# Optimization experiments

Measured on AMD Instinct MI355X. Metric: run time of the kernel, lower is better.

## Reference

```python
import math
import jax, jax.numpy as jnp
import numpy as np

T = 4096          # sequence length
H = 2048          # hidden_size
I = 8192          # intermediate_size = 4*H
LAYER_ID = 1
N_LAYERS = 24
EPS = 1e-5        # layer_norm_epsilon


def setup_inputs() -> dict:
    key = jax.random.key(0)
    ks = jax.random.split(key, 8)
    s = 1.0 / math.sqrt(H)
    si = 1.0 / math.sqrt(I)
    r0 = LAYER_ID / (N_LAYERS - 1)          # ratio_0_to_1
    r1 = 1.0 - LAYER_ID / N_LAYERS          # ratio_1_to_almost_0
    h = jnp.arange(H, dtype=jnp.float32)
    x = h / H
    time_decay = -5.0 + 8.0 * (h / (H - 1)) ** (0.7 + 1.3 * r0)
    zigzag = 0.5 * ((jnp.arange(1, H + 1) % 3).astype(jnp.float32) - 1.0)
    time_first = jnp.full((H,), math.log(0.3), jnp.float32) + zigzag
    tm_key = x ** r1
    tm_value = tm_key + 0.3 * r0
    tm_recep = x ** (0.5 * r1)
    return {
        "hidden": jax.random.normal(ks[0], (T, H), jnp.float32),
        "att_sx": jnp.zeros((H,), jnp.float32),
        "att_aa": jnp.zeros((H,), jnp.float32),
        "att_bb": jnp.zeros((H,), jnp.float32),
        "att_pp": jnp.full((H,), -1e30, jnp.float32),  # log-space -inf init
        "ffd_sx": jnp.zeros((H,), jnp.float32),
        "ln1_scale": jnp.ones((H,), jnp.float32),
        "ln1_bias": jnp.zeros((H,), jnp.float32),
        "ln2_scale": jnp.ones((H,), jnp.float32),
        "ln2_bias": jnp.zeros((H,), jnp.float32),
        "time_decay": time_decay.astype(jnp.float32),
        "time_first": time_first,
        "tm_key": tm_key.astype(jnp.float32),
        "tm_value": tm_value.astype(jnp.float32),
        "tm_recep": tm_recep.astype(jnp.float32),
        "Wk": jax.random.normal(ks[1], (H, H), jnp.float32) * s,
        "Wv": jax.random.normal(ks[2], (H, H), jnp.float32) * s,
        "Wr": jax.random.normal(ks[3], (H, H), jnp.float32) * s,
        "Wo": jax.random.normal(ks[4], (H, H), jnp.float32) * s,
        "ffn_tm_key": (x ** r1).astype(jnp.float32),
        "ffn_tm_recep": (x ** (0.5 * r1)).astype(jnp.float32),
        "Wfk": jax.random.normal(ks[5], (H, I), jnp.float32) * s,
        "Wfr": jax.random.normal(ks[6], (H, H), jnp.float32) * s,
        "Wfv": jax.random.normal(ks[7], (I, H), jnp.float32) * si,
    }


def _ln(x, scale, bias):
    mu = jnp.mean(x, axis=-1, keepdims=True)
    var = jnp.mean(jnp.square(x - mu), axis=-1, keepdims=True)
    return (x - mu) * jax.lax.rsqrt(var + EPS) * scale + bias


def _block(hidden, att_sx, att_aa, att_bb, att_pp, ffd_sx,
           ln1_scale, ln1_bias, ln2_scale, ln2_bias,
           time_decay, time_first, tm_key, tm_value, tm_recep,
           Wk, Wv, Wr, Wo, ffn_tm_key, ffn_tm_recep, Wfk, Wfr, Wfv):
    # ---- attention (WKV) sub-block ----
    x1 = _ln(hidden, ln1_scale, ln1_bias)               # [T,H]
    c_x = jnp.concatenate((att_sx[None, :], x1[:-1, :]), axis=0)  # token shift
    kx = x1 * tm_key + c_x * (1.0 - tm_key)
    vx = x1 * tm_value + c_x * (1.0 - tm_value)
    rx = x1 * tm_recep + c_x * (1.0 - tm_recep)
    r = jax.nn.sigmoid(rx @ Wr)                         # [T,H]
    k = kx @ Wk
    v = vx @ Wv
    w_decay = -jnp.exp(time_decay)                      # [H]

    def step(carry, kv):
        aa, bb, pp = carry
        kk, vv = kv
        ww = time_first + kk
        p = jnp.maximum(pp, ww)
        e1 = jnp.exp(pp - p)
        e2 = jnp.exp(ww - p)
        out_t = (e1 * aa + e2 * vv) / (e1 * bb + e2)
        ww2 = w_decay + pp
        p2 = jnp.maximum(ww2, kk)
        e1b = jnp.exp(ww2 - p2)
        e2b = jnp.exp(kk - p2)
        return (e1b * aa + e2b * vv, e1b * bb + e2b, p2), out_t

    (aa, bb, pp), cx = jax.lax.scan(step, (att_aa, att_bb, att_pp), (k, v))
    attention = x1 + (r * cx) @ Wo                      # inner residual (as in source)
    hidden2 = hidden + attention

    # ---- feed-forward (channel-mix) sub-block ----
    x2 = _ln(hidden2, ln2_scale, ln2_bias)
    sx2 = jnp.concatenate((ffd_sx[None, :], x2[:-1, :]), axis=0)
    fk = x2 * ffn_tm_key + sx2 * (1.0 - ffn_tm_key)
    fr = x2 * ffn_tm_recep + sx2 * (1.0 - ffn_tm_recep)
    rr = jax.nn.sigmoid(fr @ Wfr)
    kk2 = jnp.square(jax.nn.relu(fk @ Wfk))             # [T,I]
    ffn = rr * (kk2 @ Wfv)
    out = hidden2 + ffn
    return out, x1[-1, :], aa, bb, pp, x2[-1, :]


def reference(hidden, att_sx, att_aa, att_bb, att_pp, ffd_sx,
              ln1_scale, ln1_bias, ln2_scale, ln2_bias,
              time_decay, time_first, tm_key, tm_value, tm_recep,
              Wk, Wv, Wr, Wo, ffn_tm_key, ffn_tm_recep, Wfk, Wfr, Wfv):
    return _block(hidden, att_sx, att_aa, att_bb, att_pp, ffd_sx,
                  ln1_scale, ln1_bias, ln2_scale, ln2_bias,
                  time_decay, time_first, tm_key, tm_value, tm_recep,
                  Wk, Wv, Wr, Wo, ffn_tm_key, ffn_tm_recep, Wfk, Wfr, Wfv)
```

## Files before the change

### kernel.cpp

```cpp
#include <hip/hip_runtime.h>

#define T_SEQ 4096
#define HD 2048
#define ID 8192
#define LN_EPS 1e-5f
#define NCH 64
#define CHL 64
#define CHSZ ((size_t)NCH * HD)

typedef __attribute__((ext_vector_type(4))) float f32x4;
typedef __attribute__((ext_vector_type(8))) short short8;
typedef __attribute__((ext_vector_type(8))) unsigned short ushort8v;
typedef __attribute__((ext_vector_type(4))) unsigned short ushort4v;

#define GLB(p) ((const __attribute__((address_space(1))) void*)(p))
#define LDSP(p) ((__attribute__((address_space(3))) void*)(p))

__device__ __forceinline__ unsigned short f2bf(float f) {
  union { float f; unsigned int u; } x; x.f = f;
  unsigned int r = x.u + 0x7fffu + ((x.u >> 16) & 1u);
  return (unsigned short)(r >> 16);
}
__device__ __forceinline__ float bf2f(unsigned short u) {
  union { unsigned int i; float f; } x; x.i = ((unsigned int)u) << 16;
  return x.f;
}

__global__ void k_wt(const float* __restrict__ W, unsigned short* __restrict__ Wt,
                     int Nfull, int k_base, int n_base, int Kout) {
  __shared__ float tile[64][65];
  int tx = threadIdx.x, ty = threadIdx.y;
  int n0 = blockIdx.x * 64, k0 = blockIdx.y * 64;
#pragma unroll
  for (int j = 0; j < 8; ++j) {
    int k = ty + 8 * j;
    tile[k][tx] = W[(size_t)(k_base + k0 + k) * Nfull + n_base + n0 + tx];
  }
  __syncthreads();
  ushort8v v;
#pragma unroll
  for (int q = 0; q < 8; ++q) v[q] = f2bf(tile[ty * 8 + q][tx]);
  *(ushort8v*)&Wt[(size_t)(n0 + tx) * Kout + k0 + ty * 8] = v;
}

__global__ void k_ln(const float* __restrict__ x, const float* __restrict__ sc,
                     const float* __restrict__ bi, unsigned short* __restrict__ y,
                     float* __restrict__ lastrow) {
  int row = blockIdx.x, tid = threadIdx.x;
  const float* xr = x + (size_t)row * HD;
  f32x4 v0 = *(const f32x4*)(xr + tid * 4);
  f32x4 v1 = *(const f32x4*)(xr + 1024 + tid * 4);
  float s = 0.f, s2 = 0.f;
#pragma unroll
  for (int q = 0; q < 4; ++q) { s += v0[q] + v1[q]; s2 += v0[q] * v0[q] + v1[q] * v1[q]; }
#pragma unroll
  for (int o = 32; o; o >>= 1) { s += __shfl_xor(s, o); s2 += __shfl_xor(s2, o); }
  __shared__ float red[8];
  int wv = tid >> 6;
  if ((tid & 63) == 0) { red[wv] = s; red[4 + wv] = s2; }
  __syncthreads();
  if (tid == 0) {
    float a = red[0] + red[1] + red[2] + red[3];
    float b = red[4] + red[5] + red[6] + red[7];
    float mu = a * (1.f / HD);
    float var = b * (1.f / HD) - mu * mu;
    red[0] = mu; red[1] = rsqrtf(var + LN_EPS);
  }
  __syncthreads();
  float mu = red[0], rs = red[1];
  f32x4 s0 = *(const f32x4*)(sc + tid * 4), s1 = *(const f32x4*)(sc + 1024 + tid * 4);
  f32x4 b0 = *(const f32x4*)(bi + tid * 4), b1 = *(const f32x4*)(bi + 1024 + tid * 4);
  float o0[4], o1[4];
  ushort4v y0, y1;
#pragma unroll
  for (int q = 0; q < 4; ++q) {
    o0[q] = (v0[q] - mu) * rs * s0[q] + b0[q];
    o1[q] = (v1[q] - mu) * rs * s1[q] + b1[q];
    y0[q] = f2bf(o0[q]); y1[q] = f2bf(o1[q]);
  }
  unsigned short* yr = y + (size_t)row * HD;
  *(ushort4v*)(yr + tid * 4) = y0;
  *(ushort4v*)(yr + 1024 + tid * 4) = y1;
  if (row == T_SEQ - 1) {
#pragma unroll
    for (int q = 0; q < 4; ++q) {
      lastrow[tid * 4 + q] = o0[q];
      lastrow[1024 + tid * 4 + q] = o1[q];
    }
  }
}

__global__ void k_mix_att(const unsigned short* __restrict__ x1, const float* __restrict__ sx,
                          const float* __restrict__ tk, const float* __restrict__ tv,
                          const float* __restrict__ tr,
                          unsigned short* __restrict__ kx, unsigned short* __restrict__ vx,
                          unsigned short* __restrict__ rx) {
  size_t idx = ((size_t)blockIdx.x * 256 + threadIdx.x) * 4;
  int h = (int)(idx & (HD - 1));
  ushort4v xu = *(const ushort4v*)(x1 + idx);
  f32x4 x, c;
#pragma unroll
  for (int q = 0; q < 4; ++q) x[q] = bf2f(xu[q]);
  if (idx >= HD) {
    ushort4v cu = *(const ushort4v*)(x1 + idx - HD);
#pragma unroll
    for (int q = 0; q < 4; ++q) c[q] = bf2f(cu[q]);
  } else {
    c = *(const f32x4*)(sx + h);
  }
  f32x4 a = *(const f32x4*)(tk + h);
  f32x4 b = *(const f32x4*)(tv + h);
  f32x4 r = *(const f32x4*)(tr + h);
  ushort4v ok, ov, orr;
#pragma unroll
  for (int q = 0; q < 4; ++q) {
    ok[q] = f2bf(x[q] * a[q] + c[q] * (1.f - a[q]));
    ov[q] = f2bf(x[q] * b[q] + c[q] * (1.f - b[q]));
    orr[q] = f2bf(x[q] * r[q] + c[q] * (1.f - r[q]));
  }
  *(ushort4v*)(kx + idx) = ok;
  *(ushort4v*)(vx + idx) = ov;
  *(ushort4v*)(rx + idx) = orr;
}

__global__ void k_mix_ffn(const unsigned short* __restrict__ x2, const float* __restrict__ sx,
                          const float* __restrict__ tk, const float* __restrict__ tr,
                          unsigned short* __restrict__ fk, unsigned short* __restrict__ fr) {
  size_t idx = ((size_t)blockIdx.x * 256 + threadIdx.x) * 4;
  int h = (int)(idx & (HD - 1));
  ushort4v xu = *(const ushort4v*)(x2 + idx);
  f32x4 x, c;
#pragma unroll
  for (int q = 0; q < 4; ++q) x[q] = bf2f(xu[q]);
  if (idx >= HD) {
    ushort4v cu = *(const ushort4v*)(x2 + idx - HD);
#pragma unroll
    for (int q = 0; q < 4; ++q) c[q] = bf2f(cu[q]);
  } else {
    c = *(const f32x4*)(sx + h);
  }
  f32x4 a = *(const f32x4*)(tk + h);
  f32x4 r = *(const f32x4*)(tr + h);
  ushort4v ok, orr;
#pragma unroll
  for (int q = 0; q < 4; ++q) {
    ok[q] = f2bf(x[q] * a[q] + c[q] * (1.f - a[q]));
    orr[q] = f2bf(x[q] * r[q] + c[q] * (1.f - r[q]));
  }
  *(ushort4v*)(fk + idx) = ok;
  *(ushort4v*)(fr + idx) = orr;
}

__global__ void k_scan1(const unsigned short* __restrict__ kb,
                        const unsigned short* __restrict__ vb,
                        const float* __restrict__ td, float* __restrict__ scr) {
  int c = blockIdx.x >> 3;
  int h = (blockIdx.x & 7) * 256 + threadIdx.x;
  float wd = -__expf(td[h]);
  float a = 0.f, b = 0.f, p = -1e30f;
  size_t base = (size_t)c * CHL * HD + h;
#pragma unroll 4
  for (int u = 0; u < CHL; ++u) {
    float kk = bf2f(kb[base]), vv = bf2f(vb[base]);
    base += HD;
    float ww2 = wd + p;
    float p2 = fmaxf(ww2, kk);
    float e1 = __expf(ww2 - p2), e2 = __expf(kk - p2);
    a = e1 * a + e2 * vv;
    b = e1 * b + e2;
    p = p2;
  }
  size_t i = (size_t)c * HD + h;
  scr[i] = a;
  scr[CHSZ + i] = b;
  scr[2 * CHSZ + i] = p;
}

__global__ void k_scan2(const float* __restrict__ scr, float* __restrict__ stscr,
                        const float* __restrict__ aa0, const float* __restrict__ bb0,
                        const float* __restrict__ pp0, const float* __restrict__ td,
                        float* __restrict__ st) {
  int h = blockIdx.x * 256 + threadIdx.x;
  float aa = aa0[h], bb = bb0[h], pp = pp0[h];
  float wdL = -__expf(td[h]) * (float)CHL;
  for (int c = 0; c < NCH; ++c) {
    size_t i = (size_t)c * HD + h;
    stscr[i] = aa;
    stscr[CHSZ + i] = bb;
    stscr[2 * CHSZ + i] = pp;
    float ca = scr[i], cb = scr[CHSZ + i], cp = scr[2 * CHSZ + i];
    float ww2 = wdL + pp;
    float p2 = fmaxf(ww2, cp);
    float e1 = __expf(ww2 - p2), e2 = __expf(cp - p2);
    aa = e1 * aa + e2 * ca;
    bb = e1 * bb + e2 * cb;
    pp = p2;
  }
  st[HD + h] = aa;
  st[2 * HD + h] = bb;
  st[3 * HD + h] = pp;
}

__global__ void k_scan3(const unsigned short* __restrict__ kb,
                        const unsigned short* __restrict__ vb,
                        const unsigned short* __restrict__ rb,
                        const float* __restrict__ tf_, const float* __restrict__ td,
                        const float* __restrict__ stscr, unsigned short* __restrict__ rcx) {
  int c = blockIdx.x >> 3;
  int h = (blockIdx.x & 7) * 256 + threadIdx.x;
  size_t i0 = (size_t)c * HD + h;
  float aa = stscr[i0], bb = stscr[CHSZ + i0], pp = stscr[2 * CHSZ + i0];
  float tf = tf_[h];
  float wd = -__expf(td[h]);
  size_t base = (size_t)c * CHL * HD + h;
#pragma unroll 4
  for (int u = 0; u < CHL; ++u) {
    float kk = bf2f(kb[base]), vv = bf2f(vb[base]), rv = bf2f(rb[base]);
    float ww = tf + kk;
    float p = fmaxf(pp, ww);
    float e1 = __expf(pp - p), e2 = __expf(ww - p);
    float cx = (e1 * aa + e2 * vv) / (e1 * bb + e2);
    rcx[base] = f2bf(rv * cx);
    float ww2 = wd + pp;
    float p2 = fmaxf(ww2, kk);
    float e1b = __expf(ww2 - p2), e2b = __expf(kk - p2);
    aa = e1b * aa + e2b * vv;
    bb = e1b * bb + e2b;
    pp = p2;
    base += HD;
  }
}

__global__ void k_fvred(float* __restrict__ out, const unsigned short* __restrict__ rr,
                        const unsigned short* __restrict__ p0,
                        const unsigned short* __restrict__ p1) {
  size_t i = ((size_t)blockIdx.x * 256 + threadIdx.x) * 4;
  f32x4 o = *(f32x4*)(out + i);
  ushort4v r = *(const ushort4v*)(rr + i);
  ushort4v a = *(const ushort4v*)(p0 + i);
  ushort4v b = *(const ushort4v*)(p1 + i);
#pragma unroll
  for (int q = 0; q < 4; ++q) o[q] += bf2f(r[q]) * (bf2f(a[q]) + bf2f(b[q]));
  *(f32x4*)(out + i) = o;
}

#define MFMA_Q(mh, nh, bset)                                                   \
  _Pragma("unroll") for (int i_ = 0; i_ < 4; ++i_)                             \
  _Pragma("unroll") for (int j_ = 0; j_ < 2; ++j_)                             \
  _Pragma("unroll") for (int ks_ = 0; ks_ < 2; ++ks_)                          \
    acc[(mh)*4 + i_][(nh)*2 + j_] = __builtin_amdgcn_mfma_f32_16x16x32_bf16(   \
        aS[i_ * 2 + ks_], bset[j_ * 2 + ks_], acc[(mh)*4 + i_][(nh)*2 + j_], 0, 0, 0);

#define RD_A(mh)                                                               \
  { const char* pa_ = Ab + arow0 + (mh)*8192;                                  \
    aS[0] = *(const short8*)(pa_ + 0 * 2048 + swz0);                           \
    aS[1] = *(const short8*)(pa_ + 0 * 2048 + swz1);                           \
    aS[2] = *(const short8*)(pa_ + 1 * 2048 + swz0);                           \
    aS[3] = *(const short8*)(pa_ + 1 * 2048 + swz1);                           \
    aS[4] = *(const short8*)(pa_ + 2 * 2048 + swz0);                           \
    aS[5] = *(const short8*)(pa_ + 2 * 2048 + swz1);                           \
    aS[6] = *(const short8*)(pa_ + 3 * 2048 + swz0);                           \
    aS[7] = *(const short8*)(pa_ + 3 * 2048 + swz1); }

#define RD_B(arr, nh)                                                          \
  { const char* pb_ = Bb + brow0 + (nh)*4096;                                  \
    arr[0] = *(const short8*)(pb_ + 0 * 2048 + swz0);                          \
    arr[1] = *(const short8*)(pb_ + 0 * 2048 + swz1);                          \
    arr[2] = *(const short8*)(pb_ + 1 * 2048 + swz0);                          \
    arr[3] = *(const short8*)(pb_ + 1 * 2048 + swz1); }

template <int EPI>
__global__ __launch_bounds__(512, 2) void k_gemm256(
    const unsigned short* __restrict__ A, const unsigned short* __restrict__ A1,
    const unsigned short* __restrict__ A2,
    const unsigned short* __restrict__ Bt, const unsigned short* __restrict__ Bt1,
    const unsigned short* __restrict__ Bt2,
    int M, int N, int K, int lda, int ldb,
    unsigned short* __restrict__ Cb, unsigned short* __restrict__ Cb1,
    unsigned short* __restrict__ Cb2) {
  int koff = 0;
  if (EPI == 10) {
    koff = blockIdx.z * K;
    if (blockIdx.z) Cb = Cb1;
  } else {
    if (blockIdx.z == 1) { A = A1; Bt = Bt1; Cb = Cb1; }
    else if (blockIdx.z == 2) { A = A2; Bt = Bt2; Cb = Cb2; }
  }
  __shared__ char lds[131072];
  int tid = threadIdx.x;
  int wid = tid >> 6, lane = tid & 63;
  int row_l = lane & 15, kg = lane >> 4;
  int warp_m = wid >> 2, warp_n = wid & 3;
  int m0 = blockIdx.x * 256, n0 = blockIdx.y * 256;

  f32x4 acc[8][4];
#pragma unroll
  for (int i = 0; i < 8; ++i)
#pragma unroll
    for (int j = 0; j < 4; ++j)
#pragma unroll
      for (int q = 0; q < 4; ++q) acc[i][j][q] = 0.f;

  int srow = tid >> 3;
  int schunk = (tid & 7) ^ (srow & 7);
  const unsigned short* Asrc = A + (size_t)(m0 + srow) * lda + koff + schunk * 8;
  const unsigned short* Bsrc = Bt + (size_t)(n0 + srow) * ldb + koff + schunk * 8;
  char* ldsw = lds + wid * 1024;

  auto STAGE_A = [&](int d, int kt) {
#pragma unroll
    for (int h = 0; h < 2; ++h) {
      const unsigned short* s = Asrc + (size_t)(h * 128) * lda + kt;
      char* dst = ldsw + d * 65536 + h * 16384;
      __builtin_amdgcn_global_load_lds(GLB(s), LDSP(dst), 16, 0, 0);
      __builtin_amdgcn_global_load_lds(GLB(s + (size_t)64 * lda), LDSP(dst + 8192), 16, 0, 0);
    }
  };
  auto STAGE_B = [&](int d, int kt) {
#pragma unroll
    for (int h = 0; h < 2; ++h) {
      const unsigned short* s = Bsrc + (size_t)(h * 128) * ldb + kt;
      char* dst = ldsw + d * 65536 + 32768 + h * 16384;
      __builtin_amdgcn_global_load_lds(GLB(s), LDSP(dst), 16, 0, 0);
      __builtin_amdgcn_global_load_lds(GLB(s + (size_t)64 * ldb), LDSP(dst + 8192), 16, 0, 0);
    }
  };

  int swz0 = ((kg) ^ (row_l & 7)) << 4;
  int swz1 = ((4 + kg) ^ (row_l & 7)) << 4;
  int arow0 = (warp_m * 128 + row_l) * 128;
  int brow0 = (warp_n * 64 + row_l) * 128;

  short8 aS[8], b0[4], b1[4];
  int nt = K >> 6;
  STAGE_A(0, 0);
  STAGE_B(0, 0);

#pragma unroll 1
  for (int t = 0; t < nt; ++t) {
    int d = t & 1;
    const char* Ab = lds + d * 65536;
    const char* Bb = lds + d * 65536 + 32768;
    bool pre = (t + 1 < nt);
    int kn = (t + 1) << 6;
    if (pre) {
      STAGE_A(d ^ 1, kn);
      asm volatile("s_waitcnt vmcnt(4)" ::: "memory");
    } else {
      asm volatile("s_waitcnt vmcnt(0)" ::: "memory");
    }
    __builtin_amdgcn_s_barrier();
    RD_A(0)
    RD_B(b0, 0)
    asm volatile("s_waitcnt lgkmcnt(0)" ::: "memory");
    __builtin_amdgcn_s_setprio(1);
    MFMA_Q(0, 0, b0)
    __builtin_amdgcn_s_setprio(0);
    __builtin_amdgcn_s_barrier();
    if (pre) STAGE_B(d ^ 1, kn);
    RD_B(b1, 1)
    asm volatile("s_waitcnt lgkmcnt(0)" ::: "memory");
    __builtin_amdgcn_s_setprio(1);
    MFMA_Q(0, 1, b1)
    __builtin_amdgcn_s_setprio(0);
    __builtin_amdgcn_s_barrier();
    RD_A(1)
    asm volatile("s_waitcnt lgkmcnt(0)" ::: "memory");
    __builtin_amdgcn_s_setprio(1);
    MFMA_Q(1, 1, b1)
    __builtin_amdgcn_s_setprio(0);
    __builtin_amdgcn_s_barrier();
    __builtin_amdgcn_s_setprio(1);
    MFMA_Q(1, 0, b0)
    __builtin_amdgcn_s_setprio(0);
    __builtin_amdgcn_s_barrier();
  }

#pragma unroll
  for (int i = 0; i < 8; ++i) {
#pragma unroll
    for (int j = 0; j < 4; ++j) {
#pragma unroll
      for (int q = 0; q < 4; ++q) {
        int r = m0 + warp_m * 128 + i * 16 + kg * 4 + q;
        int c = n0 + warp_n * 64 + j * 16 + row_l;
        size_t idx = (size_t)r * N + c;
        float val = acc[i][j][q];
        if (EPI == 2) { float t2 = val > 0.f ? val * val : 0.f; Cb[idx] = f2bf(t2); }
        if (EPI == 8) {
          float o = (blockIdx.z == 2) ? 1.f / (1.f + __expf(-val)) : val;
          Cb[idx] = f2bf(o);
        }
        if (EPI == 10) Cb[idx] = f2bf(val);
      }
    }
  }
}

template <int EPI, int SWAP>
__global__ __launch_bounds__(512) void k_gemmB(
    const unsigned short* __restrict__ A, const unsigned short* __restrict__ Bt,
    int M, int N, int K, int lda, float* __restrict__ C,
    unsigned short* __restrict__ Cb, const float* __restrict__ E0,
    const unsigned short* __restrict__ E1b, const unsigned short* __restrict__ E0b) {
  __shared__ char lds[147456];
  int tid = threadIdx.x;
  int wid = tid >> 6, lane = tid & 63;
  int row_l = lane & 15, kg = lane >> 4;
  int warp_m = wid >> 2, warp_n = wid & 3;
  int bm = SWAP ? blockIdx.y : blockIdx.x;
  int bn = SWAP ? blockIdx.x : blockIdx.y;
  int m0 = bm * 128, n0 = bn * 256;

  f32x4 acc[4][4];
#pragma unroll
  for (int i = 0; i < 4; ++i)
#pragma unroll
    for (int j = 0; j < 4; ++j)
#pragma unroll
      for (int q = 0; q < 4; ++q) acc[i][j][q] = 0.f;

  int srow = tid >> 3;
  int schunk = (tid & 7) ^ (srow & 7);
  const unsigned short* Asrc = A + (size_t)(m0 + srow) * lda + schunk * 8;
  const unsigned short* Bsrc = Bt + (size_t)(n0 + srow) * K + schunk * 8;
  int wsw = wid * 1024;

  auto STAGE_P1 = [&](int d, int kt) {
    char* base = lds + d * 49152;
    __builtin_amdgcn_global_load_lds(GLB(Asrc + kt), LDSP(base + wsw), 16, 0, 0);
    __builtin_amdgcn_global_load_lds(GLB(Asrc + (size_t)64 * lda + kt),
                                     LDSP(base + 8192 + wsw), 16, 0, 0);
    __builtin_amdgcn_global_load_lds(GLB(Bsrc + kt), LDSP(base + 16384 + wsw), 16, 0, 0);
  };
  auto STAGE_P2 = [&](int d, int kt) {
    char* base = lds + d * 49152;
#pragma unroll
    for (int h = 1; h < 4; ++h)
      __builtin_amdgcn_global_load_lds(GLB(Bsrc + (size_t)(h * 64) * K + kt),
                                       LDSP(base + 16384 + h * 8192 + wsw), 16, 0, 0);
  };

  int swz0 = ((kg) ^ (row_l & 7)) << 4;
  int swz1 = ((4 + kg) ^ (row_l & 7)) << 4;
  int arow0 = (warp_m * 64 + row_l) * 128;
  int brow0 = (warp_n * 64 + row_l) * 128;

  short8 aS[8], b0[4], b1[4];
  int nt = K >> 6;
  STAGE_P1(0, 0); STAGE_P2(0, 0);
  STAGE_P1(1, 64); STAGE_P2(1, 64);

#pragma unroll 1
  for (int t = 0; t < nt; ++t) {
    int d = t % 3;
    const char* Ab = lds + d * 49152;
    const char* Bb = lds + d * 49152 + 16384;
    int b2 = t + 2 < nt ? (t + 2) % 3 : 0;
    int k2 = (t + 2) << 6;
    if (t + 2 < nt) {
      STAGE_P1(b2, k2);
      asm volatile("s_waitcnt vmcnt(9)" ::: "memory");
    } else if (t + 1 < nt) {
      asm volatile("s_waitcnt vmcnt(6)" ::: "memory");
    } else {
      asm volatile("s_waitcnt vmcnt(0)" ::: "memory");
    }
    __builtin_amdgcn_s_barrier();
    RD_A(0)
    RD_B(b0, 0)
    asm volatile("s_waitcnt lgkmcnt(0)" ::: "memory");
    __builtin_amdgcn_s_setprio(1);
    MFMA_Q(0, 0, b0)
    __builtin_amdgcn_s_setprio(0);
    __builtin_amdgcn_s_barrier();
    if (t + 2 < nt) STAGE_P2(b2, k2);
    RD_B(b1, 1)
    asm volatile("s_waitcnt lgkmcnt(0)" ::: "memory");
    __builtin_amdgcn_s_setprio(1);
    MFMA_Q(0, 1, b1)
    __builtin_amdgcn_s_setprio(0);
    __builtin_amdgcn_s_barrier();
  }

#pragma unroll
  for (int i = 0; i < 4; ++i) {
#pragma unroll
    for (int j = 0; j < 4; ++j) {
#pragma unroll
      for (int q = 0; q < 4; ++q) {
        int r = m0 + warp_m * 64 + i * 16 + kg * 4 + q;
        int c = n0 + warp_n * 64 + j * 16 + row_l;
        size_t idx = (size_t)r * N + c;
        float val = acc[i][j][q];
        if (EPI == 3) C[idx] = val + E0[idx] + bf2f(E1b[idx]);
        if (EPI == 6) Cb[idx] = f2bf(1.f / (1.f + __expf(-val)));
        if (EPI == 7) C[idx] += bf2f(E0b[idx]) * val;
      }
    }
  }
}

extern "C" void kernel_launch(void* const* d_in, const int* in_sizes, int n_in,
                              void* d_out, int out_size, void* d_ws, size_t ws_size,
                              hipStream_t stream) {
  (void)in_sizes; (void)n_in; (void)out_size;
  const float* hidden     = (const float*)d_in[0];
  const float* att_sx     = (const float*)d_in[1];
  const float* att_aa     = (const float*)d_in[2];
  const float* att_bb     = (const float*)d_in[3];
  const float* att_pp     = (const float*)d_in[4];
  const float* ffd_sx     = (const float*)d_in[5];
  const float* ln1_s      = (const float*)d_in[6];
  const float* ln1_b      = (const float*)d_in[7];
  const float* ln2_s      = (const float*)d_in[8];
  const float* ln2_b      = (const float*)d_in[9];
  const float* time_decay = (const float*)d_in[10];
  const float* time_first = (const float*)d_in[11];
  const float* tm_key     = (const float*)d_in[12];
  const float* tm_value   = (const float*)d_in[13];
  const float* tm_recep   = (const float*)d_in[14];
  const float* Wk         = (const float*)d_in[15];
  const float* Wv         = (const float*)d_in[16];
  const float* Wr         = (const float*)d_in[17];
  const float* Wo         = (const float*)d_in[18];
  const float* ffn_tm_key = (const float*)d_in[19];
  const float* ffn_tm_rec = (const float*)d_in[20];
  const float* Wfk        = (const float*)d_in[21];
  const float* Wfr        = (const float*)d_in[22];
  const float* Wfv        = (const float*)d_in[23];
  float* out = (float*)d_out;
  float* st = out + (size_t)T_SEQ * HD;

  const size_t MB8 = (size_t)HD * HD * 2;
  const size_t PG = (size_t)T_SEQ * HD * 2;
  char* w = (char*)d_ws;
  unsigned short* s0 = (unsigned short*)(w);
  unsigned short* s1 = (unsigned short*)(w + MB8);
  unsigned short* s2 = (unsigned short*)(w + 2 * MB8);
  unsigned short* s3 = (unsigned short*)(w + 3 * MB8);
  char* pA = w + 4 * MB8;
  char* pB = pA + PG;
  char* pC = pB + PG;
  char* pD = pC + PG;
  char* pE = pD + PG;
  char* pF = pE + PG;

  unsigned short* kx   = (unsigned short*)pA;
  unsigned short* vx   = (unsigned short*)pB;
  unsigned short* rx   = (unsigned short*)pC;
  unsigned short* kbf  = (unsigned short*)pD;
  unsigned short* x1bf = (unsigned short*)pE;
  unsigned short* vbf  = (unsigned short*)pF;
  unsigned short* rbf  = (unsigned short*)out;
  unsigned short* rcx  = (unsigned short*)pC;
  unsigned short* x2bf = (unsigned short*)pD;
  unsigned short* fk   = (unsigned short*)pF;
  unsigned short* fr   = (unsigned short*)pB;
  unsigned short* rr   = (unsigned short*)pA;
  unsigned short* kk2  = (unsigned short*)pB;
  unsigned short* pfv0 = (unsigned short*)pF;
  unsigned short* pfv1 = (unsigned short*)(w + 4 * MB8 + 6 * PG);
  float* scr   = (float*)s0;
  float* stscr = (float*)s1;
  bool big_ws = ws_size >= (size_t)(4 * MB8 + 7 * PG);

  dim3 tb64(64, 8);
  dim3 wg64(HD / 64, HD / 64);
  dim3 gBs(HD / 256, T_SEQ / 128);

  k_wt<<<wg64, tb64, 0, stream>>>(Wk, s0, HD, 0, 0, HD);
  k_wt<<<wg64, tb64, 0, stream>>>(Wv, s1, HD, 0, 0, HD);
  k_wt<<<wg64, tb64, 0, stream>>>(Wr, s2, HD, 0, 0, HD);
  k_wt<<<wg64, tb64, 0, stream>>>(Wo, s3, HD, 0, 0, HD);
  k_ln<<<T_SEQ, 256, 0, stream>>>(hidden, ln1_s, ln1_b, x1bf, st);
  k_mix_att<<<T_SEQ * HD / 1024, 256, 0, stream>>>(x1bf, att_sx, tm_key, tm_value, tm_recep,
                                                   kx, vx, rx);
  k_gemm256<8><<<dim3(T_SEQ / 256, HD / 256, 3), 512, 0, stream>>>(
      kx, vx, rx, s0, s1, s2, T_SEQ, HD, HD, HD, HD, kbf, vbf, rbf);
  k_scan1<<<NCH * 8, 256, 0, stream>>>(kbf, vbf, time_decay, scr);
  k_scan2<<<HD / 256, 256, 0, stream>>>(scr, stscr, att_aa, att_bb, att_pp, time_decay, st);
  k_scan3<<<NCH * 8, 256, 0, stream>>>(kbf, vbf, rbf, time_first, time_decay, stscr, rcx);
  k_gemmB<3, 1><<<gBs, 512, 0, stream>>>(rcx, s3, T_SEQ, HD, HD, HD, out, nullptr,
                                         hidden, x1bf, nullptr);

  k_ln<<<T_SEQ, 256, 0, stream>>>(out, ln2_s, ln2_b, x2bf, st + 4 * HD);
  k_mix_ffn<<<T_SEQ * HD / 1024, 256, 0, stream>>>(x2bf, ffd_sx, ffn_tm_key, ffn_tm_rec,
                                                   fk, fr);
  k_wt<<<wg64, tb64, 0, stream>>>(Wfr, s3, HD, 0, 0, HD);
  k_gemmB<6, 1><<<gBs, 512, 0, stream>>>(fr, s3, T_SEQ, HD, HD, HD, nullptr, rr,
                                         nullptr, nullptr, nullptr);
  for (int q = 0; q < 4; ++q)
    k_wt<<<wg64, tb64, 0, stream>>>(Wfk, s0 + (size_t)q * 2048 * 2048, ID, 0, q * 2048, HD);
  k_gemm256<2><<<dim3(T_SEQ / 256, ID / 256), 512, 0, stream>>>(
      fk, nullptr, nullptr, s0, nullptr, nullptr, T_SEQ, ID, HD, HD, HD,
      kk2, nullptr, nullptr);
  for (int q = 0; q < 4; ++q)
    k_wt<<<dim3(HD / 64, HD / 64), tb64, 0, stream>>>(Wfv, s0 + (size_t)q * 2048, HD,
                                                      q * 2048, 0, ID);
  if (big_ws) {
    k_gemm256<10><<<dim3(T_SEQ / 256, HD / 256, 2), 512, 0, stream>>>(
        kk2, nullptr, nullptr, s0, nullptr, nullptr, T_SEQ, HD, ID / 2, ID, ID,
        pfv0, pfv1, nullptr);
    k_fvred<<<T_SEQ * HD / 1024, 256, 0, stream>>>(out, rr, pfv0, pfv1);
  } else {
    k_gemmB<7, 1><<<gBs, 512, 0, stream>>>(kk2, s0, T_SEQ, HD, ID, ID, out, nullptr,
                                           nullptr, nullptr, rr);
  }
}
```

Baseline: 657.1 us.

## Batch weight transposes, drop gemmB block swap, fold rr scaling into split-K epilogue

The separate per-weight transpose launches are merged into batched launches that select the matrix from blockIdx.z. The transpose write-back changes from a vectorised 8-element store to coalesced scalar stores. The gemmB grid stops swapping blocks, so blockIdx.x now indexes M. The rr gate multiply moves from the reduction kernel into the split-K GEMM epilogue, which removes one read stream from the reduction but rounds each product to bf16 before the two halves are summed.

```diff
diff --git a/kernel.cpp b/kernel.cpp
--- a/kernel.cpp
+++ b/kernel.cpp
@@ -10,7 +10,6 @@
 
 typedef __attribute__((ext_vector_type(4))) float f32x4;
 typedef __attribute__((ext_vector_type(8))) short short8;
-typedef __attribute__((ext_vector_type(8))) unsigned short ushort8v;
 typedef __attribute__((ext_vector_type(4))) unsigned short ushort4v;
 
 #define GLB(p) ((const __attribute__((address_space(1))) void*)(p))
@@ -26,8 +25,9 @@
   return x.f;
 }
 
-__global__ void k_wt(const float* __restrict__ W, unsigned short* __restrict__ Wt,
-                     int Nfull, int k_base, int n_base, int Kout) {
+__device__ __forceinline__ void wt_body(const float* __restrict__ W,
+                                        unsigned short* __restrict__ Wt,
+                                        int Nfull, int k_base, int n_base, int Kout) {
   __shared__ float tile[64][65];
   int tx = threadIdx.x, ty = threadIdx.y;
   int n0 = blockIdx.x * 64, k0 = blockIdx.y * 64;
@@ -37,10 +37,31 @@
     tile[k][tx] = W[(size_t)(k_base + k0 + k) * Nfull + n_base + n0 + tx];
   }
   __syncthreads();
-  ushort8v v;
-#pragma unroll
-  for (int q = 0; q < 8; ++q) v[q] = f2bf(tile[ty * 8 + q][tx]);
-  *(ushort8v*)&Wt[(size_t)(n0 + tx) * Kout + k0 + ty * 8] = v;
+#pragma unroll
+  for (int j = 0; j < 8; ++j) {
+    int n = ty + 8 * j;
+    Wt[(size_t)(n0 + n) * Kout + k0 + tx] = f2bf(tile[tx][n]);
+  }
+}
+
+__global__ void k_wt(const float* __restrict__ W, unsigned short* __restrict__ Wt) {
+  wt_body(W, Wt, HD, 0, 0, HD);
+}
+
+__global__ void k_wt4(const float* __restrict__ W0, const float* __restrict__ W1,
+                      const float* __restrict__ W2, const float* __restrict__ W3,
+                      unsigned short* __restrict__ T) {
+  const float* W = W0;
+  if (blockIdx.z == 1) W = W1;
+  else if (blockIdx.z == 2) W = W2;
+  else if (blockIdx.z == 3) W = W3;
+  wt_body(W, T + (size_t)blockIdx.z * HD * HD, HD, 0, 0, HD);
+}
+
+__global__ void k_wtB(const float* __restrict__ W, unsigned short* __restrict__ Wt,
+                      int Nfull, int Kout, int kbz, int nbz, long dstz) {
+  int z = blockIdx.z;
+  wt_body(W, Wt + (size_t)z * dstz, Nfull, z * kbz, z * nbz, Kout);
 }
 
 __global__ void k_ln(const float* __restrict__ x, const float* __restrict__ sc,
@@ -231,16 +252,14 @@
   }
 }
 
-__global__ void k_fvred(float* __restrict__ out, const unsigned short* __restrict__ rr,
-                        const unsigned short* __restrict__ p0,
+__global__ void k_fvred(float* __restrict__ out, const unsigned short* __restrict__ p0,
                         const unsigned short* __restrict__ p1) {
   size_t i = ((size_t)blockIdx.x * 256 + threadIdx.x) * 4;
   f32x4 o = *(f32x4*)(out + i);
-  ushort4v r = *(const ushort4v*)(rr + i);
   ushort4v a = *(const ushort4v*)(p0 + i);
   ushort4v b = *(const ushort4v*)(p1 + i);
 #pragma unroll
-  for (int q = 0; q < 4; ++q) o[q] += bf2f(r[q]) * (bf2f(a[q]) + bf2f(b[q]));
+  for (int q = 0; q < 4; ++q) o[q] += bf2f(a[q]) + bf2f(b[q]);
   *(f32x4*)(out + i) = o;
 }
 
@@ -277,7 +296,7 @@
     const unsigned short* __restrict__ Bt2,
     int M, int N, int K, int lda, int ldb,
     unsigned short* __restrict__ Cb, unsigned short* __restrict__ Cb1,
-    unsigned short* __restrict__ Cb2) {
+    unsigned short* __restrict__ Cb2, const unsigned short* __restrict__ E0b) {
   int koff = 0;
   if (EPI == 10) {
     koff = blockIdx.z * K;
@@ -391,13 +410,13 @@
           float o = (blockIdx.z == 2) ? 1.f / (1.f + __expf(-val)) : val;
           Cb[idx] = f2bf(o);
         }
-        if (EPI == 10) Cb[idx] = f2bf(val);
+        if (EPI == 10) Cb[idx] = f2bf(bf2f(E0b[idx]) * val);
       }
     }
   }
 }
 
-template <int EPI, int SWAP>
+template <int EPI>
 __global__ __launch_bounds__(512) void k_gemmB(
     const unsigned short* __restrict__ A, const unsigned short* __restrict__ Bt,
     int M, int N, int K, int lda, float* __restrict__ C,
@@ -408,9 +427,7 @@
   int wid = tid >> 6, lane = tid & 63;
   int row_l = lane & 15, kg = lane >> 4;
   int warp_m = wid >> 2, warp_n = wid & 3;
-  int bm = SWAP ? blockIdx.y : blockIdx.x;
-  int bn = SWAP ? blockIdx.x : blockIdx.y;
-  int m0 = bm * 128, n0 = bn * 256;
+  int m0 = blockIdx.x * 128, n0 = blockIdx.y * 256;
 
   f32x4 acc[4][4];
 #pragma unroll
@@ -567,44 +584,39 @@
 
   dim3 tb64(64, 8);
   dim3 wg64(HD / 64, HD / 64);
-  dim3 gBs(HD / 256, T_SEQ / 128);
-
-  k_wt<<<wg64, tb64, 0, stream>>>(Wk, s0, HD, 0, 0, HD);
-  k_wt<<<wg64, tb64, 0, stream>>>(Wv, s1, HD, 0, 0, HD);
-  k_wt<<<wg64, tb64, 0, stream>>>(Wr, s2, HD, 0, 0, HD);
-  k_wt<<<wg64, tb64, 0, stream>>>(Wo, s3, HD, 0, 0, HD);
+  dim3 gB(T_SEQ / 128, HD / 256);
+
+  k_wt4<<<dim3(HD / 64, HD / 64, 4), tb64, 0, stream>>>(Wk, Wv, Wr, Wo, s0);
   k_ln<<<T_SEQ, 256, 0, stream>>>(hidden, ln1_s, ln1_b, x1bf, st);
   k_mix_att<<<T_SEQ * HD / 1024, 256, 0, stream>>>(x1bf, att_sx, tm_key, tm_value, tm_recep,
                                                    kx, vx, rx);
   k_gemm256<8><<<dim3(T_SEQ / 256, HD / 256, 3), 512, 0, stream>>>(
-      kx, vx, rx, s0, s1, s2, T_SEQ, HD, HD, HD, HD, kbf, vbf, rbf);
+      kx, vx, rx, s0, s1, s2, T_SEQ, HD, HD, HD, HD, kbf, vbf, rbf, nullptr);
   k_scan1<<<NCH * 8, 256, 0, stream>>>(kbf, vbf, time_decay, scr);
   k_scan2<<<HD / 256, 256, 0, stream>>>(scr, stscr, att_aa, att_bb, att_pp, time_decay, st);
   k_scan3<<<NCH * 8, 256, 0, stream>>>(kbf, vbf, rbf, time_first, time_decay, stscr, rcx);
-  k_gemmB<3, 1><<<gBs, 512, 0, stream>>>(rcx, s3, T_SEQ, HD, HD, HD, out, nullptr,
-                                         hidden, x1bf, nullptr);
+  k_gemmB<3><<<gB, 512, 0, stream>>>(rcx, s3, T_SEQ, HD, HD, HD, out, nullptr,
+                                     hidden, x1bf, nullptr);
 
   k_ln<<<T_SEQ, 256, 0, stream>>>(out, ln2_s, ln2_b, x2bf, st + 4 * HD);
   k_mix_ffn<<<T_SEQ * HD / 1024, 256, 0, stream>>>(x2bf, ffd_sx, ffn_tm_key, ffn_tm_rec,
                                                    fk, fr);
-  k_wt<<<wg64, tb64, 0, stream>>>(Wfr, s3, HD, 0, 0, HD);
-  k_gemmB<6, 1><<<gBs, 512, 0, stream>>>(fr, s3, T_SEQ, HD, HD, HD, nullptr, rr,
-                                         nullptr, nullptr, nullptr);
-  for (int q = 0; q < 4; ++q)
-    k_wt<<<wg64, tb64, 0, stream>>>(Wfk, s0 + (size_t)q * 2048 * 2048, ID, 0, q * 2048, HD);
+  k_wt<<<wg64, tb64, 0, stream>>>(Wfr, s3);
+  k_gemmB<6><<<gB, 512, 0, stream>>>(fr, s3, T_SEQ, HD, HD, HD, nullptr, rr,
+                                     nullptr, nullptr, nullptr);
+  k_wtB<<<dim3(HD / 64, HD / 64, 4), tb64, 0, stream>>>(Wfk, s0, ID, HD, 0, 2048,
+                                                        (long)2048 * 2048);
   k_gemm256<2><<<dim3(T_SEQ / 256, ID / 256), 512, 0, stream>>>(
       fk, nullptr, nullptr, s0, nullptr, nullptr, T_SEQ, ID, HD, HD, HD,
-      kk2, nullptr, nullptr);
-  for (int q = 0; q < 4; ++q)
-    k_wt<<<dim3(HD / 64, HD / 64), tb64, 0, stream>>>(Wfv, s0 + (size_t)q * 2048, HD,
-                                                      q * 2048, 0, ID);
+      kk2, nullptr, nullptr, nullptr);
+  k_wtB<<<dim3(HD / 64, HD / 64, 4), tb64, 0, stream>>>(Wfv, s0, HD, ID, 2048, 0, 2048);
   if (big_ws) {
     k_gemm256<10><<<dim3(T_SEQ / 256, HD / 256, 2), 512, 0, stream>>>(
         kk2, nullptr, nullptr, s0, nullptr, nullptr, T_SEQ, HD, ID / 2, ID, ID,
-        pfv0, pfv1, nullptr);
-    k_fvred<<<T_SEQ * HD / 1024, 256, 0, stream>>>(out, rr, pfv0, pfv1);
+        pfv0, pfv1, nullptr, rr);
+    k_fvred<<<T_SEQ * HD / 1024, 256, 0, stream>>>(out, pfv0, pfv1);
   } else {
-    k_gemmB<7, 1><<<gBs, 512, 0, stream>>>(kk2, s0, T_SEQ, HD, ID, ID, out, nullptr,
-                                           nullptr, nullptr, rr);
-  }
-}
+    k_gemmB<7><<<gB, 512, 0, stream>>>(kk2, s0, T_SEQ, HD, ID, ID, out, nullptr,
+                                       nullptr, nullptr, rr);
+  }
+}
```

Measured after the change: 603.1 us (median of 3 runs). 1.09x faster.
